# Kernel tuning notes

Hardware: AMD Instinct MI355X
Metric: run time of the kernel (lower is better)

## Reference

```python
import jax, jax.numpy as jnp
import numpy as np

B, TOPN, OUT, PAD, IOU_TH, IM = 16, 4, 224, 224, 0.25, 448
HP = IM + 2 * PAD  # padded image side = 896

_ANCHOR_SETTINGS = (
    dict(stride=32, size=48, scale=[2 ** (1. / 3.), 2 ** (2. / 3.)], aspect_ratio=[0.667, 1, 1.5]),
    dict(stride=64, size=96, scale=[2 ** (1. / 3.), 2 ** (2. / 3.)], aspect_ratio=[0.667, 1, 1.5]),
    dict(stride=128, size=192, scale=[1, 2 ** (1. / 3.), 2 ** (2. / 3.)], aspect_ratio=[0.667, 1, 1.5]),
)

def _edge_anchors(input_shape=(IM, IM)):
    # NTS-Net generate_default_anchor_maps: per layer, loop scale then aspect,
    # each emitting an HxW map flattened row-major -> matches tidy conv channel-major flatten.
    out = []
    for a in _ANCHOR_SETTINGS:
        st = a['stride']
        H = int(np.ceil(input_shape[0] / st)); W = int(np.ceil(input_shape[1] / st))
        cy = np.broadcast_to((np.arange(H) * st + st / 2.)[:, None], (H, W))
        cx = np.broadcast_to((np.arange(W) * st + st / 2.)[None, :], (H, W))
        for sc in a['scale']:
            for ar in a['aspect_ratio']:
                h = a['size'] * sc / np.sqrt(ar); w = a['size'] * sc * np.sqrt(ar)
                out.append(np.stack([cy - h / 2., cx - w / 2., cy + h / 2., cx + w / 2.], -1).reshape(-1, 4))
    e = np.concatenate(out, 0)
    return (e + PAD).astype(np.int32)  # module does (edge_anchors + 224).astype(int)


def _conv(x, w, b, stride, pad):
    y = jax.lax.conv_general_dilated(x, w, (stride, stride), [(pad, pad), (pad, pad)],
                                     dimension_numbers=('NCHW', 'OIHW', 'NCHW'))
    return y + b[None, :, None, None]


def _proposal_scores(rpn, w1, b1, w2, b2, w3, b3, wt1, bt1, wt2, bt2, wt3, bt3):
    d1 = jax.nn.relu(_conv(rpn, w1, b1, 1, 1))   # [B,128,14,14]
    d2 = jax.nn.relu(_conv(d1, w2, b2, 2, 1))    # [B,128,7,7]
    d3 = jax.nn.relu(_conv(d2, w3, b3, 2, 1))    # [B,128,4,4]
    bsz = rpn.shape[0]
    t1 = _conv(d1, wt1, bt1, 1, 0).reshape(bsz, -1)  # [B,1176]
    t2 = _conv(d2, wt2, bt2, 1, 0).reshape(bsz, -1)  # [B,294]
    t3 = _conv(d3, wt3, bt3, 1, 0).reshape(bsz, -1)  # [B,144]
    return jnp.concatenate([t1, t2, t3], axis=1)     # [B,1614]


def _nms_topn(scores, boxes, areas):
    # greedy hard NMS, fixed TOPN picks, suppress iou >= IOU_TH (matches upstream hard_nms)
    def step(s, _):
        i = jnp.argmax(s)
        sb = boxes[i]
        iy = jnp.clip(jnp.minimum(boxes[:, 2], sb[2]) - jnp.maximum(boxes[:, 0], sb[0]), 0.)
        ix = jnp.clip(jnp.minimum(boxes[:, 3], sb[3]) - jnp.maximum(boxes[:, 1], sb[1]), 0.)
        inter = iy * ix
        iou = inter / (areas + areas[i] - inter)
        return jnp.where(iou >= IOU_TH, -jnp.inf, s), i
    _, idxs = jax.lax.scan(step, scores, None, length=TOPN)
    return idxs  # [TOPN] int


def _crop_resize(x, anchors, top_idx):
    # batched replacement of the per-(i,j) F.interpolate(x_pad[i,:,y0:y1,x0:x1], 224, bilinear, align_corners=True)
    x_pad = jnp.pad(x, ((0, 0), (0, 0), (PAD, PAD), (PAD, PAD)))
    xp = jnp.transpose(x_pad, (0, 2, 3, 1))            # [B,HP,HP,3]
    bxs = anchors[top_idx].astype(jnp.float32)          # [B,T,4] (y0,x0,y1,x1)
    y0, x0, y1, x1 = bxs[..., 0], bxs[..., 1], bxs[..., 2], bxs[..., 3]
    t = jnp.arange(OUT, dtype=jnp.float32) / (OUT - 1)  # align_corners=True grid
    ys = y0[..., None] + t * (y1 - y0 - 1.)[..., None]  # [B,T,S] src rows in padded img
    xs = x0[..., None] + t * (x1 - x0 - 1.)[..., None]
    yi0 = jnp.floor(ys).astype(jnp.int32); yi1 = jnp.minimum(yi0 + 1, HP - 1)
    xi0 = jnp.floor(xs).astype(jnp.int32); xi1 = jnp.minimum(xi0 + 1, HP - 1)
    wy = (ys - yi0)[..., :, None, None]                 # [B,T,S,1,1]
    wx = (xs - xi0)[..., None, :, None]                 # [B,T,1,S,1]
    b = jnp.arange(x.shape[0])[:, None, None, None]
    g = lambda yi, xi: xp[b, yi[..., :, None], xi[..., None, :]]  # [B,T,S,S,3]
    v = (g(yi0, xi0) * (1 - wy) * (1 - wx) + g(yi0, xi1) * (1 - wy) * wx
         + g(yi1, xi0) * wy * (1 - wx) + g(yi1, xi1) * wy * wx)
    return jnp.transpose(v, (0, 1, 4, 2, 3))            # [B,T,3,S,S]


def setup_inputs() -> dict:
    key = jax.random.key(0)
    ks = jax.random.split(key, 16)
    he = lambda k, shape, fan: jax.random.normal(k, shape, jnp.float32) * np.sqrt(2.0 / fan)
    inp = {
        'x': jax.random.normal(ks[0], (B, 3, IM, IM), jnp.float32),
        'rpn_feature': jax.random.uniform(ks[1], (B, 2048, 14, 14), jnp.float32),
        'w_down1': he(ks[2], (128, 2048, 3, 3), 2048 * 9), 'b_down1': jnp.zeros((128,), jnp.float32),
        'w_down2': he(ks[3], (128, 128, 3, 3), 128 * 9),   'b_down2': jnp.zeros((128,), jnp.float32),
        'w_down3': he(ks[4], (128, 128, 3, 3), 128 * 9),   'b_down3': jnp.zeros((128,), jnp.float32),
        'w_tidy1': he(ks[5], (6, 128, 1, 1), 128),         'b_tidy1': jnp.zeros((6,), jnp.float32),
        'w_tidy2': he(ks[6], (6, 128, 1, 1), 128),         'b_tidy2': jnp.zeros((6,), jnp.float32),
        'w_tidy3': he(ks[7], (9, 128, 1, 1), 128),         'b_tidy3': jnp.zeros((9,), jnp.float32),
        'anchors': jnp.asarray(_edge_anchors(), jnp.int32),  # [1614,4]
    }
    return inp


def reference(x, rpn_feature, w_down1, b_down1, w_down2, b_down2, w_down3, b_down3,
              w_tidy1, b_tidy1, w_tidy2, b_tidy2, w_tidy3, b_tidy3, anchors):
    rpn_score = _proposal_scores(rpn_feature, w_down1, b_down1, w_down2, b_down2, w_down3, b_down3,
                                 w_tidy1, b_tidy1, w_tidy2, b_tidy2, w_tidy3, b_tidy3)
    boxes = anchors.astype(jnp.float32)
    areas = (boxes[:, 2] - boxes[:, 0]) * (boxes[:, 3] - boxes[:, 1])
    top_idx = jax.vmap(lambda s: _nms_topn(s, boxes, areas))(rpn_score)       # [B,TOPN]
    top_prob = jnp.take_along_axis(rpn_score, top_idx, axis=1)                # [B,TOPN]
    part_imgs = _crop_resize(x, anchors, top_idx).reshape(B * TOPN, 3, OUT, OUT)
    return part_imgs, top_idx, top_prob, rpn_score
```

## Files before the change

### kernel.cpp

```cpp
#include <hip/hip_runtime.h>
#include <math.h>

#define BATCH 16
#define TOPN 4
#define OUTS 224
#define PADW 224
#define IM 448
#define HP 896
#define NA 1614
#define IC1 2048
#define C128 128

#define N_PART (BATCH*TOPN*3*OUTS*OUTS)
#define OFF_TOPIDX  (N_PART)
#define OFF_TOPPROB (N_PART + BATCH*TOPN)
#define OFF_SCORE   (N_PART + 2*BATCH*TOPN)

#define WS_D1 0
#define WS_IDX (BATCH*C128*196)
#define WS_WT  (WS_IDX + 64)
#define NWT1 (9*2048*128)
#define NWT2 (9*128*128)
#define NRPNT (BATCH*196*IC1)

typedef __attribute__((ext_vector_type(8))) short frag8;
typedef __attribute__((ext_vector_type(16))) float acc16;
typedef __attribute__((ext_vector_type(4)))  float acc4;

__device__ __forceinline__ unsigned short f2bf(float f) {
    unsigned int u = __float_as_uint(f);
    u = (u + 0x7fffu + ((u >> 16) & 1u)) >> 16;
    return (unsigned short)u;
}
__device__ __forceinline__ float bf2f(unsigned short h) {
    return __uint_as_float(((unsigned int)h) << 16);
}
__device__ __forceinline__ void cvt4(const float* v, ushort4* h, ushort4* lo) {
    unsigned short hh[4], ll[4];
#pragma unroll
    for (int e = 0; e < 4; ++e) { hh[e] = f2bf(v[e]); ll[e] = f2bf(v[e] - bf2f(hh[e])); }
    *h  = make_ushort4(hh[0], hh[1], hh[2], hh[3]);
    *lo = make_ushort4(ll[0], ll[1], ll[2], ll[3]);
}

__device__ __forceinline__ void wrepack_body(const float* __restrict__ w,
                                             unsigned short* __restrict__ w_hi,
                                             unsigned short* __restrict__ w_lo,
                                             int IC, int i) {
    if (i >= 128 * IC) return;
    int oc = i / IC, ic = i % IC;
    const float* src = w + (size_t)(oc * IC + ic) * 9;
#pragma unroll
    for (int tap = 0; tap < 9; ++tap) {
        float v = src[tap];
        unsigned short h = f2bf(v);
        size_t gi = ((size_t)tap * 128 + oc) * IC + ic;
        w_hi[gi] = h;
        w_lo[gi] = f2bf(v - bf2f(h));
    }
}

__global__ __launch_bounds__(256) void k_prep(
    const float* __restrict__ w1, unsigned short* __restrict__ w1h, unsigned short* __restrict__ w1l,
    const float* __restrict__ w2, unsigned short* __restrict__ w2h, unsigned short* __restrict__ w2l,
    const float* __restrict__ w3, unsigned short* __restrict__ w3h, unsigned short* __restrict__ w3l,
    const float* __restrict__ rpn, unsigned short* __restrict__ TH, unsigned short* __restrict__ TL,
    const float* __restrict__ b1, float* __restrict__ d1) {
    __shared__ float tile[64 * 201];
    const int tid = threadIdx.x;
    const int blk = blockIdx.x;
    if (blk < 1024) {
        wrepack_body(w1, w1h, w1l, IC1, blk * 256 + tid);
    } else if (blk < 1088) {
        wrepack_body(w2, w2h, w2l, C128, (blk - 1024) * 256 + tid);
    } else if (blk < 1152) {
        wrepack_body(w3, w3h, w3l, C128, (blk - 1088) * 256 + tid);
    } else if (blk < 1664) {
        const int bb = blk - 1152;
        const int b = bb & 15, icg = bb >> 4;
        const int ic0 = icg * 64;
        for (int qq = tid; qq < 3136; qq += 256) {
            int icl = qq / 49, r = qq % 49, p = r * 4;
            const float4 v = *(const float4*)&rpn[(size_t)(b * IC1 + ic0 + icl) * 196 + p];
            tile[icl * 201 + p + 0] = v.x;
            tile[icl * 201 + p + 1] = v.y;
            tile[icl * 201 + p + 2] = v.z;
            tile[icl * 201 + p + 3] = v.w;
        }
        __syncthreads();
        for (int qq = tid; qq < 3136; qq += 256) {
            int px = qq >> 4, ic4 = (qq & 15) * 4;
            float vv[4];
#pragma unroll
            for (int e = 0; e < 4; ++e) vv[e] = tile[(ic4 + e) * 201 + px];
            ushort4 h4, l4; cvt4(vv, &h4, &l4);
            size_t gi = (size_t)(b * 196 + px) * IC1 + ic0 + ic4;
            *(ushort4*)&TH[gi] = h4;
            *(ushort4*)&TL[gi] = l4;
        }
    } else {
        int i = (blk - 1664) * 256 + tid;
        if (i < BATCH * C128 * 196) d1[i] = b1[i & 127];
    }
}

__global__ __launch_bounds__(512, 1) void k_conv1_mfma(const unsigned short* __restrict__ rpnTH,
                                                       const unsigned short* __restrict__ rpnTL,
                                                       const unsigned short* __restrict__ wt_hi,
                                                       const unsigned short* __restrict__ wt_lo,
                                                       float* __restrict__ d1) {
    __shared__ unsigned short inH[304 * 72];
    __shared__ unsigned short inL[304 * 72];
    __shared__ unsigned short wHs[128 * 72];
    __shared__ unsigned short wLs[128 * 72];

    const int tid = threadIdx.x;
    const int b = blockIdx.x & 15, kg = blockIdx.x >> 4;
    const int l = tid & 63, w = tid >> 6;
    const int ln = l & 31, q = l >> 5;
    const int mtw = w & 3, ntw = w >> 2;

    for (int i = tid; i < 304 * 72; i += 512) { inH[i] = 0; inL[i] = 0; }

    acc16 acc[2][2];
#pragma unroll
    for (int mt = 0; mt < 2; ++mt)
#pragma unroll
        for (int nt = 0; nt < 2; ++nt)
#pragma unroll
            for (int r = 0; r < 16; ++r) acc[mt][nt][r] = 0.f;

    int posa[2];
#pragma unroll
    for (int mt = 0; mt < 2; ++mt) {
        int px = (mtw * 2 + mt) * 32 + ln;
        posa[mt] = (px < 196) ? ((px / 14) * 16 + (px % 14)) : 256;
    }
    __syncthreads();

    for (int half = 0; half < 2; ++half) {
        const int ics = kg * 128 + half * 64;
        for (int qq = tid; qq < 3136; qq += 512) {
            int px = qq >> 4, ic4 = (qq & 15) * 4;
            size_t gi = (size_t)(b * 196 + px) * IC1 + ics + ic4;
            ushort4 h4 = *(const ushort4*)&rpnTH[gi];
            ushort4 l4 = *(const ushort4*)&rpnTL[gi];
            int pos = (px / 14 + 1) * 16 + (px % 14 + 1);
            *(ushort4*)&inH[pos * 72 + ic4] = h4;
            *(ushort4*)&inL[pos * 72 + ic4] = l4;
        }
        ushort4 pwh[4], pwl[4];
#pragma unroll
        for (int it = 0; it < 4; ++it) {
            int qq = tid + it * 512;
            int oc = qq >> 4, ic4 = (qq & 15) * 4;
            size_t gi = ((size_t)(0 * 128 + oc)) * IC1 + ics + ic4;
            pwh[it] = *(const ushort4*)&wt_hi[gi];
            pwl[it] = *(const ushort4*)&wt_lo[gi];
        }
        __syncthreads();

        for (int tap = 0; tap < 9; ++tap) {
#pragma unroll
            for (int it = 0; it < 4; ++it) {
                int qq = tid + it * 512;
                int oc = qq >> 4, ic4 = (qq & 15) * 4;
                *(ushort4*)&wHs[oc * 72 + ic4] = pwh[it];
                *(ushort4*)&wLs[oc * 72 + ic4] = pwl[it];
            }
            if (tap < 8) {
#pragma unroll
                for (int it = 0; it < 4; ++it) {
                    int qq = tid + it * 512;
                    int oc = qq >> 4, ic4 = (qq & 15) * 4;
                    size_t gi = ((size_t)((tap + 1) * 128 + oc)) * IC1 + ics + ic4;
                    pwh[it] = *(const ushort4*)&wt_hi[gi];
                    pwl[it] = *(const ushort4*)&wt_lo[gi];
                }
            }
            __syncthreads();

            const int off = (tap / 3) * 16 + (tap % 3);
#pragma unroll
            for (int c = 0; c < 4; ++c) {
                const int ko = c * 16 + q * 8;
                frag8 aH[2], aL[2], bH[2], bL[2];
#pragma unroll
                for (int mt = 0; mt < 2; ++mt) {
                    int pp = (posa[mt] + off) * 72 + ko;
                    aH[mt] = *(const frag8*)&inH[pp];
                    aL[mt] = *(const frag8*)&inL[pp];
                }
#pragma unroll
                for (int nt = 0; nt < 2; ++nt) {
                    int oc = (ntw * 2 + nt) * 32 + ln;
                    bH[nt] = *(const frag8*)&wHs[oc * 72 + ko];
                    bL[nt] = *(const frag8*)&wLs[oc * 72 + ko];
                }
#pragma unroll
                for (int mt = 0; mt < 2; ++mt)
#pragma unroll
                    for (int nt = 0; nt < 2; ++nt) {
                        acc[mt][nt] = __builtin_amdgcn_mfma_f32_32x32x16_bf16(aH[mt], bH[nt], acc[mt][nt], 0, 0, 0);
                        acc[mt][nt] = __builtin_amdgcn_mfma_f32_32x32x16_bf16(aH[mt], bL[nt], acc[mt][nt], 0, 0, 0);
                        acc[mt][nt] = __builtin_amdgcn_mfma_f32_32x32x16_bf16(aL[mt], bH[nt], acc[mt][nt], 0, 0, 0);
                    }
            }
            __syncthreads();
        }
    }

#pragma unroll
    for (int mt = 0; mt < 2; ++mt)
#pragma unroll
        for (int nt = 0; nt < 2; ++nt) {
            int oc = (ntw * 2 + nt) * 32 + ln;
#pragma unroll
            for (int r = 0; r < 16; ++r) {
                int m = (r & 3) + 8 * (r >> 2) + 4 * q;
                int px = (mtw * 2 + mt) * 32 + m;
                if (px < 196)
                    atomicAdd(&d1[(size_t)(b * 196 + px) * 128 + oc], acc[mt][nt][r]);
            }
        }
}

__global__ __launch_bounds__(512, 1) void k_tail(
    const float* __restrict__ d1,
    const unsigned short* __restrict__ w2h, const unsigned short* __restrict__ w2l,
    const unsigned short* __restrict__ w3h, const unsigned short* __restrict__ w3l,
    const float* __restrict__ b2, const float* __restrict__ b3,
    const float* __restrict__ wt1, const float* __restrict__ bt1,
    const float* __restrict__ wt2, const float* __restrict__ bt2,
    const float* __restrict__ wt3, const float* __restrict__ bt3,
    const int* __restrict__ anchors,
    float* __restrict__ score_out, float* __restrict__ out_idx,
    float* __restrict__ out_prob, int* __restrict__ idx_ws) {
    extern __shared__ char smem[];
    unsigned short* inH = (unsigned short*)(smem);
    unsigned short* inL = (unsigned short*)(smem + 43776);
    unsigned short* wHs = (unsigned short*)(smem + 87552);
    unsigned short* wLs = (unsigned short*)(smem + 105984);
    unsigned short* t1H = (unsigned short*)(smem + 124416);
    unsigned short* t1L = (unsigned short*)(smem + 126720);
    float*  d2f  = (float*)(smem + 129024);
    float*  sbuf = (float*)(smem + 154112);
    unsigned short* dhH = (unsigned short*)(smem);
    unsigned short* dhL = (unsigned short*)(smem + 27648);
    float*  d3f  = (float*)(smem + 55296);
    unsigned short* t2H = (unsigned short*)(smem + 63488);
    unsigned short* t2L = (unsigned short*)(smem + 65792);
    unsigned short* w3H = (unsigned short*)(smem + 68096);
    unsigned short* w3L = (unsigned short*)(smem + 86528);
    float* wt3s = (float*)(smem);
    float* y0s = (float*)(smem + 6464);
    float* x0s = (float*)(smem + 12928);
    float* y1s = (float*)(smem + 19392);
    float* x1s = (float*)(smem + 25856);
    float* ars = (float*)(smem + 32320);
    float* rv  = (float*)(smem + 38784);
    int*   ri  = (int*)(smem + 39808);

    const int tid = threadIdx.x;
    const int b = blockIdx.x;
    const int l = tid & 63, w = tid >> 6;
    const int ln = l & 31, q = l >> 5;
    const int l16 = l & 15, q4 = l >> 4;

    for (int i = tid; i < 304 * 72; i += 512) { inH[i] = 0; inL[i] = 0; }

    acc16 c2;
    acc4 t1a[2];
#pragma unroll
    for (int r = 0; r < 16; ++r) c2[r] = 0.f;
#pragma unroll
    for (int i = 0; i < 2; ++i)
#pragma unroll
        for (int r = 0; r < 4; ++r) t1a[i][r] = 0.f;

    const int mtw = w & 1, ntw = w >> 1;
    int posa2;
    {
        int px = mtw * 32 + ln;
        posa2 = (px < 49) ? ((px / 7) * 32 + (px % 7) * 2) : 256;
    }
    __syncthreads();

    for (int half = 0; half < 2; ++half) {
        const int ics = half * 64;
        for (int qq = tid; qq < 3136; qq += 512) {
            int px = qq >> 4, ic4 = (qq & 15) * 4;
            float4 v = *(const float4*)&d1[(size_t)(b * 196 + px) * 128 + ics + ic4];
            float vv[4] = {fmaxf(v.x, 0.f), fmaxf(v.y, 0.f), fmaxf(v.z, 0.f), fmaxf(v.w, 0.f)};
            ushort4 h4, l4; cvt4(vv, &h4, &l4);
            int pos = (px / 14 + 1) * 16 + (px % 14 + 1);
            *(ushort4*)&inH[pos * 72 + ic4] = h4;
            *(ushort4*)&inL[pos * 72 + ic4] = l4;
        }
        for (int qq = tid; qq < 1024; qq += 512) {
            int m = qq >> 6, k = qq & 63;
            float v = (m < 6) ? wt1[m * 128 + ics + k] : 0.f;
            unsigned short h = f2bf(v);
            t1H[m * 72 + k] = h;
            t1L[m * 72 + k] = f2bf(v - bf2f(h));
        }
        ushort4 pwh[4], pwl[4];
#pragma unroll
        for (int it = 0; it < 4; ++it) {
            int qq = tid + it * 512;
            int oc = qq >> 4, ic4 = (qq & 15) * 4;
            size_t gi = ((size_t)(0 * 128 + oc)) * C128 + ics + ic4;
            pwh[it] = *(const ushort4*)&w2h[gi];
            pwl[it] = *(const ushort4*)&w2l[gi];
        }
        __syncthreads();

        for (int tap = 0; tap < 9; ++tap) {
#pragma unroll
            for (int it = 0; it < 4; ++it) {
                int qq = tid + it * 512;
                int oc = qq >> 4, ic4 = (qq & 15) * 4;
                *(ushort4*)&wHs[oc * 72 + ic4] = pwh[it];
                *(ushort4*)&wLs[oc * 72 + ic4] = pwl[it];
            }
            if (tap < 8) {
#pragma unroll
                for (int it = 0; it < 4; ++it) {
                    int qq = tid + it * 512;
                    int oc = qq >> 4, ic4 = (qq & 15) * 4;
                    size_t gi = ((size_t)((tap + 1) * 128 + oc)) * C128 + ics + ic4;
                    pwh[it] = *(const ushort4*)&w2h[gi];
                    pwl[it] = *(const ushort4*)&w2l[gi];
                }
            }
            __syncthreads();
            const int off = (tap / 3) * 16 + (tap % 3);
#pragma unroll
            for (int c = 0; c < 4; ++c) {
                const int ko = c * 16 + q * 8;
                int pp = (posa2 + off) * 72 + ko;
                frag8 aH = *(const frag8*)&inH[pp];
                frag8 aL = *(const frag8*)&inL[pp];
                int oc = ntw * 32 + ln;
                frag8 bH = *(const frag8*)&wHs[oc * 72 + ko];
                frag8 bL = *(const frag8*)&wLs[oc * 72 + ko];
                c2 = __builtin_amdgcn_mfma_f32_32x32x16_bf16(aH, bH, c2, 0, 0, 0);
                c2 = __builtin_amdgcn_mfma_f32_32x32x16_bf16(aH, bL, c2, 0, 0, 0);
                c2 = __builtin_amdgcn_mfma_f32_32x32x16_bf16(aL, bH, c2, 0, 0, 0);
            }
            __syncthreads();
        }

#pragma unroll
        for (int i = 0; i < 2; ++i) {
            int px = (w * 2 + i) * 16 + l16;
            int pos = (px < 196) ? ((px / 14 + 1) * 16 + (px % 14 + 1)) : 256;
#pragma unroll
            for (int c = 0; c < 2; ++c) {
                int ko = c * 32 + q4 * 8;
                frag8 aH = *(const frag8*)&t1H[l16 * 72 + ko];
                frag8 aL = *(const frag8*)&t1L[l16 * 72 + ko];
                frag8 bH = *(const frag8*)&inH[pos * 72 + ko];
                frag8 bL = *(const frag8*)&inL[pos * 72 + ko];
                t1a[i] = __builtin_amdgcn_mfma_f32_16x16x32_bf16(aH, bH, t1a[i], 0, 0, 0);
                t1a[i] = __builtin_amdgcn_mfma_f32_16x16x32_bf16(aH, bL, t1a[i], 0, 0, 0);
                t1a[i] = __builtin_amdgcn_mfma_f32_16x16x32_bf16(aL, bH, t1a[i], 0, 0, 0);
            }
        }
        __syncthreads();
    }

    {
        int oc = ntw * 32 + ln;
        float bias = b2[oc];
#pragma unroll
        for (int r = 0; r < 16; ++r) {
            int m = (r & 3) + 8 * (r >> 2) + 4 * q;
            int px = mtw * 32 + m;
            if (px < 49) d2f[px * 128 + oc] = fmaxf(c2[r] + bias, 0.f);
        }
    }
#pragma unroll
    for (int i = 0; i < 2; ++i) {
        int px = (w * 2 + i) * 16 + l16;
#pragma unroll
        for (int r = 0; r < 4; ++r) {
            int oc = q4 * 4 + r;
            if (oc < 6 && px < 196) {
                float v = t1a[i][r] + bt1[oc];
                sbuf[oc * 196 + px] = v;
                score_out[b * NA + oc * 196 + px] = v;
            }
        }
    }
    __syncthreads();

    for (int i = tid; i < 192 * 72; i += 512) { dhH[i] = 0; dhL[i] = 0; }

    acc16 c3;
    acc4 t2a;
#pragma unroll
    for (int r = 0; r < 16; ++r) c3[r] = 0.f;
#pragma unroll
    for (int r = 0; r < 4; ++r) t2a[r] = 0.f;

    const int posb3 = (ln < 16) ? ((ln / 4) * 32 + (ln % 4) * 2) : 144;
    const int pxt2 = (w - 4) * 16 + l16;
    const int posbt2 = (w >= 4 && pxt2 < 49) ? ((pxt2 / 7 + 1) * 16 + (pxt2 % 7 + 1)) : 144;
    __syncthreads();

    for (int half = 0; half < 2; ++half) {
        const int ics = half * 64;
        for (int qq = tid; qq < 784; qq += 512) {
            int px = qq >> 4, ic4 = (qq & 15) * 4;
            float4 v = *(const float4*)&d2f[px * 128 + ics + ic4];
            float vv[4] = {v.x, v.y, v.z, v.w};
            ushort4 h4, l4; cvt4(vv, &h4, &l4);
            int pos = (px / 7 + 1) * 16 + (px % 7 + 1);
            *(ushort4*)&dhH[pos * 72 + ic4] = h4;
            *(ushort4*)&dhL[pos * 72 + ic4] = l4;
        }
        for (int qq = tid; qq < 1024; qq += 512) {
            int m = qq >> 6, k = qq & 63;
            float v = (m < 6) ? wt2[m * 128 + ics + k] : 0.f;
            unsigned short h = f2bf(v);
            t2H[m * 72 + k] = h;
            t2L[m * 72 + k] = f2bf(v - bf2f(h));
        }
        ushort4 pwh[4], pwl[4];
#pragma unroll
        for (int it = 0; it < 4; ++it) {
            int qq = tid + it * 512;
            int oc = qq >> 4, ic4 = (qq & 15) * 4;
            size_t gi = ((size_t)(0 * 128 + oc)) * C128 + ics + ic4;
            pwh[it] = *(const ushort4*)&w3h[gi];
            pwl[it] = *(const ushort4*)&w3l[gi];
        }
        __syncthreads();

        for (int tap = 0; tap < 9; ++tap) {
#pragma unroll
            for (int it = 0; it < 4; ++it) {
                int qq = tid + it * 512;
                int oc = qq >> 4, ic4 = (qq & 15) * 4;
                *(ushort4*)&w3H[oc * 72 + ic4] = pwh[it];
                *(ushort4*)&w3L[oc * 72 + ic4] = pwl[it];
            }
            if (tap < 8) {
#pragma unroll
                for (int it = 0; it < 4; ++it) {
                    int qq = tid + it * 512;
                    int oc = qq >> 4, ic4 = (qq & 15) * 4;
                    size_t gi = ((size_t)((tap + 1) * 128 + oc)) * C128 + ics + ic4;
                    pwh[it] = *(const ushort4*)&w3h[gi];
                    pwl[it] = *(const ushort4*)&w3l[gi];
                }
            }
            __syncthreads();
            const int off = (tap / 3) * 16 + (tap % 3);
            if (w < 4) {
#pragma unroll
                for (int c = 0; c < 4; ++c) {
                    const int ko = c * 16 + q * 8;
                    int pp = (posb3 + off) * 72 + ko;
                    frag8 aH = *(const frag8*)&dhH[pp];
                    frag8 aL = *(const frag8*)&dhL[pp];
                    int oc = w * 32 + ln;
                    frag8 bH = *(const frag8*)&w3H[oc * 72 + ko];
                    frag8 bL = *(const frag8*)&w3L[oc * 72 + ko];
                    c3 = __builtin_amdgcn_mfma_f32_32x32x16_bf16(aH, bH, c3, 0, 0, 0);
                    c3 = __builtin_amdgcn_mfma_f32_32x32x16_bf16(aH, bL, c3, 0, 0, 0);
                    c3 = __builtin_amdgcn_mfma_f32_32x32x16_bf16(aL, bH, c3, 0, 0, 0);
                }
            } else if (tap == 0) {
#pragma unroll
                for (int c = 0; c < 2; ++c) {
                    int ko = c * 32 + q4 * 8;
                    frag8 aH = *(const frag8*)&t2H[l16 * 72 + ko];
                    frag8 aL = *(const frag8*)&t2L[l16 * 72 + ko];
                    frag8 bH = *(const frag8*)&dhH[posbt2 * 72 + ko];
                    frag8 bL = *(const frag8*)&dhL[posbt2 * 72 + ko];
                    t2a = __builtin_amdgcn_mfma_f32_16x16x32_bf16(aH, bH, t2a, 0, 0, 0);
                    t2a = __builtin_amdgcn_mfma_f32_16x16x32_bf16(aH, bL, t2a, 0, 0, 0);
                    t2a = __builtin_amdgcn_mfma_f32_16x16x32_bf16(aL, bH, t2a, 0, 0, 0);
                }
            }
            __syncthreads();
        }
    }

    if (w < 4) {
        int oc = w * 32 + ln;
        float bias = b3[oc];
#pragma unroll
        for (int r = 0; r < 16; ++r) {
            int px = (r & 3) + 8 * (r >> 2) + 4 * q;
            if (px < 16) d3f[oc * 16 + px] = fmaxf(c3[r] + bias, 0.f);
        }
    } else {
#pragma unroll
        for (int r = 0; r < 4; ++r) {
            int oc = q4 * 4 + r;
            if (oc < 6 && pxt2 < 49) {
                float v = t2a[r] + bt2[oc];
                sbuf[1176 + oc * 49 + pxt2] = v;
                score_out[b * NA + 1176 + oc * 49 + pxt2] = v;
            }
        }
    }
    for (int i = tid; i < 1152; i += 512) wt3s[i] = wt3[i];
    __syncthreads();

    if (tid < 144) {
        int oc = tid >> 4, px = tid & 15;
        float s = bt3[oc];
        for (int ic = 0; ic < 128; ++ic) s += wt3s[oc * 128 + ic] * d3f[ic * 16 + px];
        sbuf[1470 + oc * 16 + px] = s;
        score_out[b * NA + 1470 + oc * 16 + px] = s;
    }
    for (int j = tid; j < NA; j += 512) {
        int4 a = ((const int4*)anchors)[j];
        float a0 = (float)a.x, a1 = (float)a.y, a2 = (float)a.z, a3 = (float)a.w;
        y0s[j] = a0; x0s[j] = a1; y1s[j] = a2; x1s[j] = a3;
        ars[j] = (a2 - a0) * (a3 - a1);
    }
    __syncthreads();

    for (int it = 0; it < TOPN; ++it) {
        float bv = -INFINITY; int bi = NA;
        for (int j = tid; j < NA; j += 512) {
            float v = sbuf[j];
            if (v > bv || (v == bv && j < bi)) { bv = v; bi = j; }
        }
#pragma unroll
        for (int d = 1; d < 64; d <<= 1) {
            float ov = __shfl_xor(bv, d, 64);
            int   oi = __shfl_xor(bi, d, 64);
            if (ov > bv || (ov == bv && oi < bi)) { bv = ov; bi = oi; }
        }
        if (l == 0) { rv[w] = bv; ri[w] = bi; }
        __syncthreads();
        if (tid == 0) {
            float V = rv[0]; int K = ri[0];
#pragma unroll
            for (int j = 1; j < 8; ++j) {
                float ov = rv[j]; int oi = ri[j];
                if (ov > V || (ov == V && oi < K)) { V = ov; K = oi; }
            }
            ri[8] = K;
            out_idx[b * TOPN + it] = (float)K;
            out_prob[b * TOPN + it] = V;
            idx_ws[b * TOPN + it] = K;
        }
        __syncthreads();
        int K = ri[8];
        float ky0 = y0s[K], kx0 = x0s[K], ky1 = y1s[K], kx1 = x1s[K], ka = ars[K];
        for (int j = tid; j < NA; j += 512) {
            float iy = fmaxf(fminf(y1s[j], ky1) - fmaxf(y0s[j], ky0), 0.f);
            float ix = fmaxf(fminf(x1s[j], kx1) - fmaxf(x0s[j], kx0), 0.f);
            float inter = iy * ix;
            float iou = inter / (ars[j] + ka - inter);
            if (iou >= 0.25f) sbuf[j] = -INFINITY;
        }
        __syncthreads();
    }
}

__global__ __launch_bounds__(256) void k_crop(const float* __restrict__ x,
                                              const int* __restrict__ anchors,
                                              const int* __restrict__ idx_ws,
                                              float* __restrict__ out) {
    int blk = blockIdx.x;
    int crop = blk / OUTS;
    int i = blk % OUTS;
    int j = threadIdx.x;
    if (j >= OUTS) return;
    int b = crop >> 2;
    int a = idx_ws[crop];
    int y0 = anchors[a * 4], x0 = anchors[a * 4 + 1];
    int y1 = anchors[a * 4 + 2], x1 = anchors[a * 4 + 3];

    float ti = (float)i / 223.f;
    float ys = (float)y0 + ti * (float)(y1 - y0 - 1);
    int yi0 = (int)ys;
    int yi1 = min(yi0 + 1, HP - 1);
    float wy = ys - (float)yi0;

    float tj = (float)j / 223.f;
    float xs = (float)x0 + tj * (float)(x1 - x0 - 1);
    int xi0 = (int)xs;
    int xi1 = min(xi0 + 1, HP - 1);
    float wx = xs - (float)xi0;

    int ry0 = yi0 - PADW, ry1 = yi1 - PADW, rx0 = xi0 - PADW, rx1 = xi1 - PADW;
    bool vy0 = (ry0 >= 0) && (ry0 < IM), vy1 = (ry1 >= 0) && (ry1 < IM);
    bool vx0 = (rx0 >= 0) && (rx0 < IM), vx1 = (rx1 >= 0) && (rx1 < IM);

    float w00 = (1.f - wy) * (1.f - wx), w01 = (1.f - wy) * wx;
    float w10 = wy * (1.f - wx), w11 = wy * wx;

#pragma unroll
    for (int c = 0; c < 3; ++c) {
        const float* xp = x + (size_t)(b * 3 + c) * IM * IM;
        float g00 = (vy0 && vx0) ? xp[ry0 * IM + rx0] : 0.f;
        float g01 = (vy0 && vx1) ? xp[ry0 * IM + rx1] : 0.f;
        float g10 = (vy1 && vx0) ? xp[ry1 * IM + rx0] : 0.f;
        float g11 = (vy1 && vx1) ? xp[ry1 * IM + rx1] : 0.f;
        out[(size_t)(crop * 3 + c) * OUTS * OUTS + i * OUTS + j] =
            g00 * w00 + g01 * w01 + g10 * w10 + g11 * w11;
    }
}

extern "C" void kernel_launch(void* const* d_in, const int* in_sizes, int n_in,
                              void* d_out, int out_size, void* d_ws, size_t ws_size,
                              hipStream_t stream) {
    (void)in_sizes; (void)n_in; (void)out_size; (void)ws_size;
    const float* x    = (const float*)d_in[0];
    const float* rpn  = (const float*)d_in[1];
    const float* w1   = (const float*)d_in[2];
    const float* b1   = (const float*)d_in[3];
    const float* w2   = (const float*)d_in[4];
    const float* b2   = (const float*)d_in[5];
    const float* w3   = (const float*)d_in[6];
    const float* b3   = (const float*)d_in[7];
    const float* wt1  = (const float*)d_in[8];
    const float* bt1  = (const float*)d_in[9];
    const float* wt2  = (const float*)d_in[10];
    const float* bt2  = (const float*)d_in[11];
    const float* wt3  = (const float*)d_in[12];
    const float* bt3  = (const float*)d_in[13];
    const int*   anc  = (const int*)d_in[14];

    float* out = (float*)d_out;
    float* ws  = (float*)d_ws;
    float* d1  = ws + WS_D1;
    int*   idxw = (int*)(ws + WS_IDX);
    unsigned short* w1h = (unsigned short*)(ws + WS_WT);
    unsigned short* w1l = w1h + NWT1;
    unsigned short* w2h = w1l + NWT1;
    unsigned short* w2l = w2h + NWT2;
    unsigned short* w3h = w2l + NWT2;
    unsigned short* w3l = w3h + NWT2;
    unsigned short* rpnTH = w3l + NWT2;
    unsigned short* rpnTL = rpnTH + NRPNT;

    static const int TAIL_LDS = 160568;
    hipFuncSetAttribute((const void*)k_tail, hipFuncAttributeMaxDynamicSharedMemorySize, TAIL_LDS);

    k_prep<<<3232, 256, 0, stream>>>(w1, w1h, w1l, w2, w2h, w2l, w3, w3h, w3l,
                                     rpn, rpnTH, rpnTL, b1, d1);
    k_conv1_mfma<<<256, 512, 0, stream>>>(rpnTH, rpnTL, w1h, w1l, d1);
    k_tail<<<BATCH, 512, TAIL_LDS, stream>>>(d1, w2h, w2l, w3h, w3l, b2, b3,
                                             wt1, bt1, wt2, bt2, wt3, bt3, anc,
                                             out + OFF_SCORE, out + OFF_TOPIDX,
                                             out + OFF_TOPPROB, idxw);
    k_crop<<<BATCH * TOPN * OUTS, 256, 0, stream>>>(x, anc, idxw, out);
}
```

Before: 289.5 us.

## Prepack conv1 weights into MFMA fragment order and load B operands directly from global

The weight repack for conv1 now writes the bf16 hi/lo weights in MFMA B-fragment order, so each lane can fetch its 8-element fragment with one contiguous vector load. The conv1 kernel drops the LDS staging of weights and the per-tap barriers, reading B fragments straight from global/L2 inside a fully unrolled tap loop. It also shrinks the padded input LDS buffer, widens the input loads to 8 elements, and swaps the block-index mapping so consecutive blocks share a batch. The cost is more global load traffic per wave for weights, which now depends on cache hits, and higher register pressure from the unrolled loop.

```diff
diff --git a/kernel.cpp b/kernel.cpp
--- a/kernel.cpp
+++ b/kernel.cpp
@@ -60,6 +60,33 @@
     }
 }
 
+__device__ __forceinline__ void w1frag_body(const float* __restrict__ w1,
+                                            unsigned short* __restrict__ w1h,
+                                            unsigned short* __restrict__ w1l,
+                                            int i) {
+    if (i >= 9 * 32768) return;
+    int l  = i & 63;
+    int ot = (i >> 6) & 3;
+    int c  = (i >> 8) & 3;
+    int h  = (i >> 10) & 1;
+    int kg = (i >> 11) & 15;
+    int t  = i >> 15;
+    int oc  = ot * 32 + (l & 31);
+    int ic0 = kg * 128 + h * 64 + c * 16 + (l >> 5) * 8;
+    const float* src = w1 + ((size_t)oc * IC1 + ic0) * 9 + t;
+    frag8 hv, lv;
+#pragma unroll
+    for (int e = 0; e < 8; ++e) {
+        float v = src[e * 9];
+        unsigned short hs = f2bf(v);
+        hv[e] = (short)hs;
+        lv[e] = (short)f2bf(v - bf2f(hs));
+    }
+    size_t dst = (size_t)i * 8;
+    *(frag8*)&w1h[dst] = hv;
+    *(frag8*)&w1l[dst] = lv;
+}
+
 __global__ __launch_bounds__(256) void k_prep(
     const float* __restrict__ w1, unsigned short* __restrict__ w1h, unsigned short* __restrict__ w1l,
     const float* __restrict__ w2, unsigned short* __restrict__ w2h, unsigned short* __restrict__ w2l,
@@ -69,14 +96,14 @@
     __shared__ float tile[64 * 201];
     const int tid = threadIdx.x;
     const int blk = blockIdx.x;
-    if (blk < 1024) {
-        wrepack_body(w1, w1h, w1l, IC1, blk * 256 + tid);
-    } else if (blk < 1088) {
-        wrepack_body(w2, w2h, w2l, C128, (blk - 1024) * 256 + tid);
-    } else if (blk < 1152) {
-        wrepack_body(w3, w3h, w3l, C128, (blk - 1088) * 256 + tid);
-    } else if (blk < 1664) {
-        const int bb = blk - 1152;
+    if (blk < 1152) {
+        w1frag_body(w1, w1h, w1l, blk * 256 + tid);
+    } else if (blk < 1216) {
+        wrepack_body(w2, w2h, w2l, C128, (blk - 1152) * 256 + tid);
+    } else if (blk < 1280) {
+        wrepack_body(w3, w3h, w3l, C128, (blk - 1216) * 256 + tid);
+    } else if (blk < 1792) {
+        const int bb = blk - 1280;
         const int b = bb & 15, icg = bb >> 4;
         const int ic0 = icg * 64;
         for (int qq = tid; qq < 3136; qq += 256) {
@@ -99,28 +126,26 @@
             *(ushort4*)&TL[gi] = l4;
         }
     } else {
-        int i = (blk - 1664) * 256 + tid;
+        int i = (blk - 1792) * 256 + tid;
         if (i < BATCH * C128 * 196) d1[i] = b1[i & 127];
     }
 }
 
 __global__ __launch_bounds__(512, 1) void k_conv1_mfma(const unsigned short* __restrict__ rpnTH,
                                                        const unsigned short* __restrict__ rpnTL,
-                                                       const unsigned short* __restrict__ wt_hi,
-                                                       const unsigned short* __restrict__ wt_lo,
+                                                       const unsigned short* __restrict__ wfh,
+                                                       const unsigned short* __restrict__ wfl,
                                                        float* __restrict__ d1) {
-    __shared__ unsigned short inH[304 * 72];
-    __shared__ unsigned short inL[304 * 72];
-    __shared__ unsigned short wHs[128 * 72];
-    __shared__ unsigned short wLs[128 * 72];
+    __shared__ unsigned short inH[256 * 72];
+    __shared__ unsigned short inL[256 * 72];
 
     const int tid = threadIdx.x;
-    const int b = blockIdx.x & 15, kg = blockIdx.x >> 4;
+    const int b = blockIdx.x >> 4, kg = blockIdx.x & 15;
     const int l = tid & 63, w = tid >> 6;
     const int ln = l & 31, q = l >> 5;
     const int mtw = w & 3, ntw = w >> 2;
 
-    for (int i = tid; i < 304 * 72; i += 512) { inH[i] = 0; inL[i] = 0; }
+    for (int i = tid; i < 256 * 72; i += 512) { inH[i] = 0; inL[i] = 0; }
 
     acc16 acc[2][2];
 #pragma unroll
@@ -134,57 +159,42 @@
 #pragma unroll
     for (int mt = 0; mt < 2; ++mt) {
         int px = (mtw * 2 + mt) * 32 + ln;
-        posa[mt] = (px < 196) ? ((px / 14) * 16 + (px % 14)) : 256;
-    }
+        posa[mt] = (px < 196) ? ((px / 14) * 16 + (px % 14)) : 0;
+    }
+
+    const size_t wb0 = (size_t)kg * 16384 + (size_t)l * 8;
     __syncthreads();
 
     for (int half = 0; half < 2; ++half) {
         const int ics = kg * 128 + half * 64;
-        for (int qq = tid; qq < 3136; qq += 512) {
-            int px = qq >> 4, ic4 = (qq & 15) * 4;
-            size_t gi = (size_t)(b * 196 + px) * IC1 + ics + ic4;
-            ushort4 h4 = *(const ushort4*)&rpnTH[gi];
-            ushort4 l4 = *(const ushort4*)&rpnTL[gi];
+        for (int qq = tid; qq < 1568; qq += 512) {
+            int px = qq >> 3, ic8 = (qq & 7) * 8;
+            size_t gi = (size_t)(b * 196 + px) * IC1 + ics + ic8;
+            frag8 h8 = *(const frag8*)&rpnTH[gi];
+            frag8 l8 = *(const frag8*)&rpnTL[gi];
             int pos = (px / 14 + 1) * 16 + (px % 14 + 1);
-            *(ushort4*)&inH[pos * 72 + ic4] = h4;
-            *(ushort4*)&inL[pos * 72 + ic4] = l4;
-        }
-        ushort4 pwh[4], pwl[4];
-#pragma unroll
-        for (int it = 0; it < 4; ++it) {
-            int qq = tid + it * 512;
-            int oc = qq >> 4, ic4 = (qq & 15) * 4;
-            size_t gi = ((size_t)(0 * 128 + oc)) * IC1 + ics + ic4;
-            pwh[it] = *(const ushort4*)&wt_hi[gi];
-            pwl[it] = *(const ushort4*)&wt_lo[gi];
-        }
-        __syncthreads();
-
+            *(frag8*)&inH[pos * 72 + ic8] = h8;
+            *(frag8*)&inL[pos * 72 + ic8] = l8;
+        }
+        __syncthreads();
+
+        const size_t wbh = wb0 + (size_t)half * 8192;
+#pragma unroll
         for (int tap = 0; tap < 9; ++tap) {
-#pragma unroll
-            for (int it = 0; it < 4; ++it) {
-                int qq = tid + it * 512;
-                int oc = qq >> 4, ic4 = (qq & 15) * 4;
-                *(ushort4*)&wHs[oc * 72 + ic4] = pwh[it];
-                *(ushort4*)&wLs[oc * 72 + ic4] = pwl[it];
-            }
-            if (tap < 8) {
-#pragma unroll
-                for (int it = 0; it < 4; ++it) {
-                    int qq = tid + it * 512;
-                    int oc = qq >> 4, ic4 = (qq & 15) * 4;
-                    size_t gi = ((size_t)((tap + 1) * 128 + oc)) * IC1 + ics + ic4;
-                    pwh[it] = *(const ushort4*)&wt_hi[gi];
-                    pwl[it] = *(const ushort4*)&wt_lo[gi];
+            const unsigned short* WH = wfh + wbh + (size_t)tap * 262144;
+            const unsigned short* WL = wfl + wbh + (size_t)tap * 262144;
+            const int off = (tap / 3) * 16 + (tap % 3);
+#pragma unroll
+            for (int c = 0; c < 4; ++c) {
+                frag8 bH[2], bL[2];
+#pragma unroll
+                for (int nt = 0; nt < 2; ++nt) {
+                    const int o2 = c * 2048 + (ntw * 2 + nt) * 512;
+                    bH[nt] = *(const frag8*)&WH[o2];
+                    bL[nt] = *(const frag8*)&WL[o2];
                 }
-            }
-            __syncthreads();
-
-            const int off = (tap / 3) * 16 + (tap % 3);
-#pragma unroll
-            for (int c = 0; c < 4; ++c) {
                 const int ko = c * 16 + q * 8;
-                frag8 aH[2], aL[2], bH[2], bL[2];
+                frag8 aH[2], aL[2];
 #pragma unroll
                 for (int mt = 0; mt < 2; ++mt) {
                     int pp = (posa[mt] + off) * 72 + ko;
@@ -192,12 +202,6 @@
                     aL[mt] = *(const frag8*)&inL[pp];
                 }
 #pragma unroll
-                for (int nt = 0; nt < 2; ++nt) {
-                    int oc = (ntw * 2 + nt) * 32 + ln;
-                    bH[nt] = *(const frag8*)&wHs[oc * 72 + ko];
-                    bL[nt] = *(const frag8*)&wLs[oc * 72 + ko];
-                }
-#pragma unroll
                 for (int mt = 0; mt < 2; ++mt)
 #pragma unroll
                     for (int nt = 0; nt < 2; ++nt) {
@@ -206,8 +210,8 @@
                         acc[mt][nt] = __builtin_amdgcn_mfma_f32_32x32x16_bf16(aL[mt], bH[nt], acc[mt][nt], 0, 0, 0);
                     }
             }
-            __syncthreads();
-        }
+        }
+        __syncthreads();
     }
 
 #pragma unroll
@@ -647,7 +651,7 @@
     static const int TAIL_LDS = 160568;
     hipFuncSetAttribute((const void*)k_tail, hipFuncAttributeMaxDynamicSharedMemorySize, TAIL_LDS);
 
-    k_prep<<<3232, 256, 0, stream>>>(w1, w1h, w1l, w2, w2h, w2l, w3, w3h, w3l,
+    k_prep<<<3360, 256, 0, stream>>>(w1, w1h, w1l, w2, w2h, w2l, w3, w3h, w3l,
                                      rpn, rpnTH, rpnTL, b1, d1);
     k_conv1_mfma<<<256, 512, 0, stream>>>(rpnTH, rpnTL, w1h, w1l, d1);
     k_tail<<<BATCH, 512, TAIL_LDS, stream>>>(d1, w2h, w2l, w3h, w3l, b2, b3,
```

New measurement: 291.7 us. About the same (+0.8%).
